# Performance work log

Hardware: AMD Instinct MI355X
Metric: run time of the kernel (lower is better)

Reference implementation:

```python
import jax, jax.numpy as jnp
import numpy as np

RESOLUTIONS = [33, 65, 129, 257, 513]
BAL = 0.5
K_CONFLICT = 3  # fixed unrolled conflict-resolution passes per level


def _up2(x):
    """Exact 2x-1 bilinear upsample with align_corners=True. [H,W]->[2H-1,2W-1]."""
    H, W = x.shape
    y = jnp.zeros((2 * H - 1, W), x.dtype)
    y = y.at[::2].set(x).at[1::2].set(0.5 * (x[:-1] + x[1:]))
    z = jnp.zeros((2 * H - 1, 2 * W - 1), x.dtype)
    z = z.at[:, ::2].set(y).at[:, 1::2].set(0.5 * (y[:, :-1] + y[:, 1:]))
    return z


def _any3x3(mask):
    """3x3 'smooth conv > 0' == any neighbor true. bool [H,W] -> bool [H,W]."""
    x = mask.astype(jnp.float32)[None, None]
    k = jnp.ones((1, 1, 3, 3), jnp.float32)
    y = jax.lax.conv_general_dilated(x, k, (1, 1), ((1, 1), (1, 1)))
    return y[0, 0] > 0


def setup_inputs() -> dict:
    key = jax.random.key(0)
    ks = jax.random.split(key, 4)
    d = 128
    return {
        "W1": jax.random.normal(ks[0], (2, d), jnp.float32) * 1.0,
        "b1": jnp.zeros((d,), jnp.float32),
        "W2": jax.random.normal(ks[1], (d, d), jnp.float32) / np.sqrt(d),
        "b2": jnp.zeros((d,), jnp.float32),
        "W3": jax.random.normal(ks[2], (d, 1), jnp.float32) * (2.0 / np.sqrt(d)),
        "b3": jnp.zeros((1,), jnp.float32),
        "b_min": jnp.zeros((2,), jnp.float32),
        "b_max": jnp.ones((2,), jnp.float32),
    }


def reference(W1, b1, W2, b2, W3, b3, b_min, b_max):
    def eval_grid(H, W):
        # align_corners=True: grid coords / (res-1) in [0,1], identical at every level
        u = jnp.linspace(0.0, 1.0, W, dtype=jnp.float32)
        v = jnp.linspace(0.0, 1.0, H, dtype=jnp.float32)
        X, Y = jnp.meshgrid(u, v)          # [H,W] each
        pts = jnp.stack([X, Y], -1).reshape(-1, 2)
        pts = b_min + pts * (b_max - b_min)
        h = jnp.tanh(pts @ W1 + b1)
        h = jnp.tanh(h @ W2 + b2)
        return jax.nn.sigmoid(h @ W3 + b3).reshape(H, W)

    Rf = RESOLUTIONS[-1]
    R0 = RESOLUTIONS[0]
    occ = eval_grid(R0, R0)                       # level-0 full evaluation
    calc = jnp.zeros((Rf, Rf), bool)
    s0 = (Rf - 1) // (R0 - 1)
    calc = calc.at[::s0, ::s0].set(True)

    for R in RESOLUTIONS[1:]:
        s = (Rf - 1) // (R - 1)
        occ_i = _up2(occ)                          # bilinear interp, align_corners=True
        valid = _up2((occ > BAL).astype(occ.dtype))
        boundary = (valid > 0) & (valid < 1)       # crossing band
        boundary = _any3x3(boundary)               # smooth_conv3x3 > 0
        calc_lvl = calc[::s, ::s]
        boundary = boundary & ~calc_lvl            # exclude already-evaluated points
        q = eval_grid(R, R)                        # query_func on level grid (masked use)
        conflicts = boundary & ((occ_i - BAL) * (q - BAL) < 0)
        occ = jnp.where(boundary, q, occ_i)        # scatter query values at boundary
        calc_lvl = calc_lvl | boundary
        # conflict resolution: re-evaluate 8-neighborhood of conflicting points
        for _ in range(K_CONFLICT):
            cand = _any3x3(conflicts) & ~calc_lvl
            conflicts = cand & ((occ - BAL) * (q - BAL) < 0)
            occ = jnp.where(cand, q, occ)
            calc_lvl = calc_lvl | cand
        calc = calc.at[::s, ::s].set(calc_lvl)

    return occ[None, None]                         # [1, 1, Rf, Rf]
```

## Files before the change

kernel.cpp:

```cpp
#include <hip/hip_runtime.h>

typedef unsigned char u8;
typedef float f32x4 __attribute__((ext_vector_type(4)));
typedef _Float16 f16x8 __attribute__((ext_vector_type(8)));

#define DIM 128
#define TM  128

__device__ __forceinline__ float fast_tanh(float x) {
    float e = __builtin_amdgcn_exp2f(x * 2.885390081777927f);
    return 1.0f - 2.0f * __builtin_amdgcn_rcpf(e + 1.0f);
}
__device__ __forceinline__ float fast_sigmoid(float x) {
    float e = __builtin_amdgcn_exp2f(x * -1.4426950408889634f);
    return __builtin_amdgcn_rcpf(1.0f + e);
}

__global__ __launch_bounds__(256, 4) void eval_q4(
    const float* __restrict__ W1, const float* __restrict__ b1,
    const float* __restrict__ W2, const float* __restrict__ b2,
    const float* __restrict__ W3, const float* __restrict__ b3,
    const float* __restrict__ bmin, const float* __restrict__ bmax,
    float* __restrict__ q4)
{
    __shared__ __align__(16) _Float16 sW2T[DIM * DIM];

    const int R = 513;
    const int N = R * R;
    const int tid = threadIdx.x;
    const int m0 = blockIdx.x * TM;

    #pragma unroll
    for (int s = 0; s < 8; ++s) {
        int chunk = s * 256 + tid;
        int n = chunk & 127, ko = chunk >> 7;
        f16x8 v;
        #pragma unroll
        for (int qq = 0; qq < 8; ++qq)
            v[qq] = (_Float16)W2[(ko * 8 + qq) * DIM + n];
        int slot = ko ^ (n & 15);
        *(f16x8*)&sW2T[n * DIM + slot * 8] = v;
    }

    const int w = tid >> 6, lane = tid & 63;
    const int l15 = lane & 15, lg = lane >> 4;

    const float inv = 1.0f / 512.0f;
    const float bx0 = bmin[0], by0 = bmin[1];
    const float sx = bmax[0] - bx0, sy = bmax[1] - by0;
    float xs[2], ys[2];
    #pragma unroll
    for (int mf = 0; mf < 2; ++mf) {
        int pi = m0 + w * 32 + mf * 16 + l15;
        int pg = (pi < N) ? pi : N - 1;
        int gi = pg / R, gj = pg - gi * R;
        xs[mf] = bx0 + (float)gj * inv * sx;
        ys[mf] = by0 + (float)gi * inv * sy;
    }

    f32x4 acc[2][8];
    #pragma unroll
    for (int nf = 0; nf < 8; ++nf) {
        float b2v = b2[nf * 16 + l15];
        acc[0][nf] = (f32x4)(b2v);
        acc[1][nf] = (f32x4)(b2v);
    }

    __syncthreads();

    #pragma unroll
    for (int kf = 0; kf < 4; ++kf) {
        const int kbase = kf * 32 + lg * 8;
        f16x8 bh[8];
        #pragma unroll
        for (int nf = 0; nf < 8; ++nf) {
            int c = nf * 16 + l15;
            int slot = (kf * 4 + lg) ^ l15;
            bh[nf] = *(const f16x8*)&sW2T[c * DIM + slot * 8];
        }
        f32x4 wxa = *(const f32x4*)&W1[kbase];
        f32x4 wxb = *(const f32x4*)&W1[kbase + 4];
        f32x4 wya = *(const f32x4*)&W1[DIM + kbase];
        f32x4 wyb = *(const f32x4*)&W1[DIM + kbase + 4];
        f32x4 b1a = *(const f32x4*)&b1[kbase];
        f32x4 b1b = *(const f32x4*)&b1[kbase + 4];
        f16x8 ah[2];
        #pragma unroll
        for (int mf = 0; mf < 2; ++mf) {
            float x = xs[mf], y = ys[mf];
            #pragma unroll
            for (int qq = 0; qq < 4; ++qq)
                ah[mf][qq] = (_Float16)fast_tanh(fmaf(x, wxa[qq], fmaf(y, wya[qq], b1a[qq])));
            #pragma unroll
            for (int qq = 0; qq < 4; ++qq)
                ah[mf][4 + qq] = (_Float16)fast_tanh(fmaf(x, wxb[qq], fmaf(y, wyb[qq], b1b[qq])));
        }
        #pragma unroll
        for (int nf = 0; nf < 8; ++nf)
            #pragma unroll
            for (int mf = 0; mf < 2; ++mf)
                acc[mf][nf] = __builtin_amdgcn_mfma_f32_16x16x32_f16(ah[mf], bh[nf], acc[mf][nf], 0, 0, 0);
    }

    float rs[2][4] = {{0,0,0,0},{0,0,0,0}};
    #pragma unroll
    for (int nf = 0; nf < 8; ++nf) {
        float w3v = W3[nf * 16 + l15];
        #pragma unroll
        for (int mf = 0; mf < 2; ++mf)
            #pragma unroll
            for (int rg = 0; rg < 4; ++rg)
                rs[mf][rg] += fast_tanh(acc[mf][nf][rg]) * w3v;
    }
    #pragma unroll
    for (int mf = 0; mf < 2; ++mf)
        #pragma unroll
        for (int rg = 0; rg < 4; ++rg) {
            float v = rs[mf][rg];
            v += __shfl_xor(v, 1);
            v += __shfl_xor(v, 2);
            v += __shfl_xor(v, 4);
            v += __shfl_xor(v, 8);
            rs[mf][rg] = v;
        }
    if (l15 == 0) {
        float b3v = b3[0];
        #pragma unroll
        for (int mf = 0; mf < 2; ++mf)
            #pragma unroll
            for (int rg = 0; rg < 4; ++rg) {
                int po = m0 + w * 32 + mf * 16 + lg * 4 + rg;
                if (po < N) q4[po] = fast_sigmoid(rs[mf][rg] + b3v);
            }
    }
}

template<int TS, int NT>
__global__ __launch_bounds__(NT) void level_kernel(
    const float* __restrict__ occP, int opRow, int opCol,
    const u8* __restrict__ calcP, int Rp,
    const float* __restrict__ q4, int qRow, int qCol,
    float* __restrict__ occOut, u8* __restrict__ calcOut, int R)
{
    constexpr int HW = TS + 8;
    __shared__ u8 sRaw[HW * HW], sCfA[HW * HW], sCfB[HW * HW];
    const int nT = (R + TS - 1) / TS;
    const int bi = blockIdx.x / nT, bj = blockIdx.x - bi * nT;
    const int fi0 = bi * TS - 4, fj0 = bj * TS - 4;
    const int c = threadIdx.x;
    const int li = c / HW, lj = c - li * HW;
    const int fi = fi0 + li, fj = fj0 + lj;
    const bool inG = (fi >= 0 && fi < R && fj >= 0 && fj < R);
    const float BAL = 0.5f;

    float occ = 0.5f, qv = 0.5f;
    u8 rw = 0; bool cal = false;
    if (inG) qv = q4[fi * qRow + fj * qCol];
    if (inG) {
        int ip = fi >> 1, jp = fj >> 1;
        float tl = occP[ip * opRow + jp * opCol];
        int oi = fi & 1, oj = fj & 1;
        bool b;
        if (!oi && !oj) { occ = tl; b = false; }
        else if (oi && !oj) {
            float bl = occP[(ip + 1) * opRow + jp * opCol];
            occ = 0.5f * (tl + bl);
            b = (tl > BAL) != (bl > BAL);
        } else if (!oi && oj) {
            float tr = occP[ip * opRow + (jp + 1) * opCol];
            occ = 0.5f * (tl + tr);
            b = (tl > BAL) != (tr > BAL);
        } else {
            float bl = occP[(ip + 1) * opRow + jp * opCol];
            float tr = occP[ip * opRow + (jp + 1) * opCol];
            float br = occP[(ip + 1) * opRow + (jp + 1) * opCol];
            occ = 0.5f * (0.5f * (tl + bl) + 0.5f * (tr + br));
            bool m0 = tl > BAL, m1 = bl > BAL, m2 = tr > BAL, m3 = br > BAL;
            b = (m0 | m1 | m2 | m3) && !(m0 & m1 & m2 & m3);
        }
        rw = b ? 1 : 0;
        if (((fi | fj) & 1) == 0) cal = calcP ? (calcP[ip * Rp + jp] != 0) : true;
    }
    sRaw[c] = rw; sCfA[c] = 0; sCfB[c] = 0;

    if (__syncthreads_or(rw)) {
        u8 cf = 0;
        if (li >= 1 && li < HW - 1 && lj >= 1 && lj < HW - 1 && inG) {
            bool b = false;
            #pragma unroll
            for (int di = -1; di <= 1; ++di)
                #pragma unroll
                for (int dj = -1; dj <= 1; ++dj)
                    if (sRaw[(li + di) * HW + (lj + dj)]) b = true;
            b = b && !cal;
            cf = (b && (occ - BAL) * (qv - BAL) < 0.0f) ? 1 : 0;
            if (b) { occ = qv; cal = true; }
            sCfA[c] = cf;
        }
        int haveCf = __syncthreads_or((int)cf);

        #pragma unroll
        for (int it = 0; it < 3; ++it) {
            if (!haveCf) break;
            const u8* cin = (it & 1) ? sCfB : sCfA;
            u8* cout      = (it & 1) ? sCfA : sCfB;
            int lo = 2 + it, hi = HW - 2 - it;
            u8 nc = 0;
            if (li >= lo && li < hi && lj >= lo && lj < hi && inG) {
                bool any = false;
                #pragma unroll
                for (int di = -1; di <= 1; ++di)
                    #pragma unroll
                    for (int dj = -1; dj <= 1; ++dj)
                        if (cin[(li + di) * HW + (lj + dj)]) any = true;
                bool cand = any && !cal;
                nc = (cand && (occ - BAL) * (qv - BAL) < 0.0f) ? 1 : 0;
                if (cand) { occ = qv; cal = true; }
                cout[c] = nc;
            }
            haveCf = __syncthreads_or((int)nc);
        }
    }

    if (li >= 4 && li < HW - 4 && lj >= 4 && lj < HW - 4 && inG) {
        occOut[fi * R + fj] = occ;
        calcOut[fi * R + fj] = cal ? 1 : 0;
    }
}

extern "C" void kernel_launch(void* const* d_in, const int* in_sizes, int n_in,
                              void* d_out, int out_size, void* d_ws, size_t ws_size,
                              hipStream_t stream) {
    const float* W1   = (const float*)d_in[0];
    const float* b1   = (const float*)d_in[1];
    const float* W2   = (const float*)d_in[2];
    const float* b2   = (const float*)d_in[3];
    const float* W3   = (const float*)d_in[4];
    const float* b3   = (const float*)d_in[5];
    const float* bmin = (const float*)d_in[6];
    const float* bmax = (const float*)d_in[7];

    const int RF = 513, N513 = RF * RF;

    float* q4   = (float*)d_ws;
    float* occA = q4 + N513;
    float* occB = occA + N513;
    u8* calcA = (u8*)(occB + N513);
    u8* calcB = calcA + N513;
    float* out = (float*)d_out;

    eval_q4<<<(N513 + TM - 1) / TM, 256, 0, stream>>>(
        W1, b1, W2, b2, W3, b3, bmin, bmax, q4);

    level_kernel<8, 256><<<81, 256, 0, stream>>>(
        q4, RF * 16, 16, (const u8*)nullptr, 33,
        q4, RF * 8, 8, occA, calcB, 65);
    level_kernel<24, 1024><<<36, 1024, 0, stream>>>(
        occA, 65, 1, calcB, 65,
        q4, RF * 4, 4, occB, calcA, 129);
    level_kernel<24, 1024><<<121, 1024, 0, stream>>>(
        occB, 129, 1, calcA, 129,
        q4, RF * 2, 2, occA, calcB, 257);
    level_kernel<24, 1024><<<484, 1024, 0, stream>>>(
        occA, 257, 1, calcB, 257,
        q4, RF, 1, out, calcA, 513);
}
```

Measured before the change: 50.42 us.

## Fuse four level kernels into one tile kernel with recomputed shrinking halos

Replaces the four per-level launches with a single kernel. Each 16x16 output tile recomputes its pyramid ancestry in a 24x24 window and passes occupancy and calc state between levels through shared memory instead of global buffers. This removes three kernel launches and the global round trips of occ/calc, at the cost of redundant halo recomputation across tiles and 576-thread blocks. Correctness depends on the halo margins at each level being wide enough for the 4-pass dilation chain.

```diff
diff --git a/kernel.cpp b/kernel.cpp
--- a/kernel.cpp
+++ b/kernel.cpp
@@ -135,63 +135,65 @@
     }
 }
 
-template<int TS, int NT>
-__global__ __launch_bounds__(NT) void level_kernel(
-    const float* __restrict__ occP, int opRow, int opCol,
-    const u8* __restrict__ calcP, int Rp,
-    const float* __restrict__ q4, int qRow, int qCol,
-    float* __restrict__ occOut, u8* __restrict__ calcOut, int R)
+#define HWF 24
+#define NTF 576
+template<bool FIRST>
+__device__ __forceinline__ void run_level(
+    int c, int li, int lj, int oi0, int oj0, int R, int qs,
+    const float* __restrict__ q4, int pOi, int pOj,
+    const float* sOccP, const u8* sCalP,
+    u8* sRaw, u8* sCfA, u8* sCfB,
+    float& occR, bool& calR)
 {
-    constexpr int HW = TS + 8;
-    __shared__ u8 sRaw[HW * HW], sCfA[HW * HW], sCfB[HW * HW];
-    const int nT = (R + TS - 1) / TS;
-    const int bi = blockIdx.x / nT, bj = blockIdx.x - bi * nT;
-    const int fi0 = bi * TS - 4, fj0 = bj * TS - 4;
-    const int c = threadIdx.x;
-    const int li = c / HW, lj = c - li * HW;
-    const int fi = fi0 + li, fj = fj0 + lj;
+    const float BAL = 0.5f;
+    const int fi = oi0 + li, fj = oj0 + lj;
     const bool inG = (fi >= 0 && fi < R && fj >= 0 && fj < R);
-    const float BAL = 0.5f;
-
     float occ = 0.5f, qv = 0.5f;
     u8 rw = 0; bool cal = false;
-    if (inG) qv = q4[fi * qRow + fj * qCol];
+    if (inG) qv = q4[(fi * qs) * 513 + fj * qs];
     if (inG) {
         int ip = fi >> 1, jp = fj >> 1;
-        float tl = occP[ip * opRow + jp * opCol];
         int oi = fi & 1, oj = fj & 1;
+        float tl = FIRST ? q4[(ip * 16) * 513 + jp * 16]
+                         : sOccP[(ip - pOi) * HWF + (jp - pOj)];
         bool b;
         if (!oi && !oj) { occ = tl; b = false; }
         else if (oi && !oj) {
-            float bl = occP[(ip + 1) * opRow + jp * opCol];
+            float bl = FIRST ? q4[((ip + 1) * 16) * 513 + jp * 16]
+                             : sOccP[(ip + 1 - pOi) * HWF + (jp - pOj)];
             occ = 0.5f * (tl + bl);
             b = (tl > BAL) != (bl > BAL);
         } else if (!oi && oj) {
-            float tr = occP[ip * opRow + (jp + 1) * opCol];
+            float tr = FIRST ? q4[(ip * 16) * 513 + (jp + 1) * 16]
+                             : sOccP[(ip - pOi) * HWF + (jp + 1 - pOj)];
             occ = 0.5f * (tl + tr);
             b = (tl > BAL) != (tr > BAL);
         } else {
-            float bl = occP[(ip + 1) * opRow + jp * opCol];
-            float tr = occP[ip * opRow + (jp + 1) * opCol];
-            float br = occP[(ip + 1) * opRow + (jp + 1) * opCol];
+            float bl = FIRST ? q4[((ip + 1) * 16) * 513 + jp * 16]
+                             : sOccP[(ip + 1 - pOi) * HWF + (jp - pOj)];
+            float tr = FIRST ? q4[(ip * 16) * 513 + (jp + 1) * 16]
+                             : sOccP[(ip - pOi) * HWF + (jp + 1 - pOj)];
+            float br = FIRST ? q4[((ip + 1) * 16) * 513 + (jp + 1) * 16]
+                             : sOccP[(ip + 1 - pOi) * HWF + (jp + 1 - pOj)];
             occ = 0.5f * (0.5f * (tl + bl) + 0.5f * (tr + br));
             bool m0 = tl > BAL, m1 = bl > BAL, m2 = tr > BAL, m3 = br > BAL;
             b = (m0 | m1 | m2 | m3) && !(m0 & m1 & m2 & m3);
         }
         rw = b ? 1 : 0;
-        if (((fi | fj) & 1) == 0) cal = calcP ? (calcP[ip * Rp + jp] != 0) : true;
+        if (((fi | fj) & 1) == 0)
+            cal = FIRST ? true : (sCalP[(ip - pOi) * HWF + (jp - pOj)] != 0);
     }
     sRaw[c] = rw; sCfA[c] = 0; sCfB[c] = 0;
 
     if (__syncthreads_or(rw)) {
         u8 cf = 0;
-        if (li >= 1 && li < HW - 1 && lj >= 1 && lj < HW - 1 && inG) {
+        if (li >= 1 && li < HWF - 1 && lj >= 1 && lj < HWF - 1 && inG) {
             bool b = false;
             #pragma unroll
             for (int di = -1; di <= 1; ++di)
                 #pragma unroll
                 for (int dj = -1; dj <= 1; ++dj)
-                    if (sRaw[(li + di) * HW + (lj + dj)]) b = true;
+                    if (sRaw[(li + di) * HWF + (lj + dj)]) b = true;
             b = b && !cal;
             cf = (b && (occ - BAL) * (qv - BAL) < 0.0f) ? 1 : 0;
             if (b) { occ = qv; cal = true; }
@@ -204,7 +206,7 @@
             if (!haveCf) break;
             const u8* cin = (it & 1) ? sCfB : sCfA;
             u8* cout      = (it & 1) ? sCfA : sCfB;
-            int lo = 2 + it, hi = HW - 2 - it;
+            int lo = 2 + it, hi = HWF - 2 - it;
             u8 nc = 0;
             if (li >= lo && li < hi && lj >= lo && lj < hi && inG) {
                 bool any = false;
@@ -212,7 +214,7 @@
                 for (int di = -1; di <= 1; ++di)
                     #pragma unroll
                     for (int dj = -1; dj <= 1; ++dj)
-                        if (cin[(li + di) * HW + (lj + dj)]) any = true;
+                        if (cin[(li + di) * HWF + (lj + dj)]) any = true;
                 bool cand = any && !cal;
                 nc = (cand && (occ - BAL) * (qv - BAL) < 0.0f) ? 1 : 0;
                 if (cand) { occ = qv; cal = true; }
@@ -221,11 +223,41 @@
             haveCf = __syncthreads_or((int)nc);
         }
     }
-
-    if (li >= 4 && li < HW - 4 && lj >= 4 && lj < HW - 4 && inG) {
-        occOut[fi * R + fj] = occ;
-        calcOut[fi * R + fj] = cal ? 1 : 0;
-    }
+    occR = occ; calR = cal;
+}
+
+__global__ __launch_bounds__(NTF) void levels_fused(
+    const float* __restrict__ q4, float* __restrict__ out)
+{
+    __shared__ float sOcc[NTF];
+    __shared__ u8 sCal[NTF], sRaw[NTF], sCfA[NTF], sCfB[NTF];
+    const int bi = blockIdx.x / 33, bj = blockIdx.x - bi * 33;
+    const int c = threadIdx.x;
+    const int li = c / HWF, lj = c - li * HWF;
+    float occ; bool cal;
+
+    run_level<true>(c, li, lj, 2 * bi - 8, 2 * bj - 8, 65, 8,
+                    q4, 0, 0, sOcc, sCal, sRaw, sCfA, sCfB, occ, cal);
+    sOcc[c] = occ; sCal[c] = cal ? 1 : 0;
+    __syncthreads();
+    run_level<false>(c, li, lj, 4 * bi - 7, 4 * bj - 7, 129, 4,
+                     q4, 2 * bi - 8, 2 * bj - 8, sOcc, sCal,
+                     sRaw, sCfA, sCfB, occ, cal);
+    sOcc[c] = occ; sCal[c] = cal ? 1 : 0;
+    __syncthreads();
+    run_level<false>(c, li, lj, 8 * bi - 6, 8 * bj - 6, 257, 2,
+                     q4, 4 * bi - 7, 4 * bj - 7, sOcc, sCal,
+                     sRaw, sCfA, sCfB, occ, cal);
+    sOcc[c] = occ; sCal[c] = cal ? 1 : 0;
+    __syncthreads();
+    run_level<false>(c, li, lj, 16 * bi - 4, 16 * bj - 4, 513, 1,
+                     q4, 8 * bi - 6, 8 * bj - 6, sOcc, sCal,
+                     sRaw, sCfA, sCfB, occ, cal);
+
+    const int fi = 16 * bi - 4 + li, fj = 16 * bj - 4 + lj;
+    if (li >= 4 && li < 20 && lj >= 4 && lj < 20 &&
+        fi < 513 && fj < 513)
+        out[fi * 513 + fj] = occ;
 }
 
 extern "C" void kernel_launch(void* const* d_in, const int* in_sizes, int n_in,
@@ -240,28 +272,12 @@
     const float* bmin = (const float*)d_in[6];
     const float* bmax = (const float*)d_in[7];
 
-    const int RF = 513, N513 = RF * RF;
-
-    float* q4   = (float*)d_ws;
-    float* occA = q4 + N513;
-    float* occB = occA + N513;
-    u8* calcA = (u8*)(occB + N513);
-    u8* calcB = calcA + N513;
+    const int N513 = 513 * 513;
+    float* q4  = (float*)d_ws;
     float* out = (float*)d_out;
 
     eval_q4<<<(N513 + TM - 1) / TM, 256, 0, stream>>>(
         W1, b1, W2, b2, W3, b3, bmin, bmax, q4);
 
-    level_kernel<8, 256><<<81, 256, 0, stream>>>(
-        q4, RF * 16, 16, (const u8*)nullptr, 33,
-        q4, RF * 8, 8, occA, calcB, 65);
-    level_kernel<24, 1024><<<36, 1024, 0, stream>>>(
-        occA, 65, 1, calcB, 65,
-        q4, RF * 4, 4, occB, calcA, 129);
-    level_kernel<24, 1024><<<121, 1024, 0, stream>>>(
-        occB, 129, 1, calcA, 129,
-        q4, RF * 2, 2, occA, calcB, 257);
-    level_kernel<24, 1024><<<484, 1024, 0, stream>>>(
-        occA, 257, 1, calcB, 257,
-        q4, RF, 1, out, calcA, 513);
-}
+    levels_fused<<<33 * 33, NTF, 0, stream>>>(q4, out);
+}
```

Result: faster. 46.95 us (-6.9%).
